# Performance work log

Hardware: AMD Instinct MI355X
Metric: run time of the kernel (lower is better)

Reference implementation:

```python
import jax, jax.numpy as jnp
import numpy as np

N_BUILD = 200000
N_COMM = 10000
E_BUILD = 1200000
E_COMM = 160000
D_B = 64    # building feature dim
D_C = 32    # community feature dim
H = 64      # hidden dim (comm embedding)
D_FUSE = D_B + H  # 128
N_CLS = 2


def gcn(x, src, dst, W, b):
    """PyG-style GCNConv with self-loops and symmetric normalization.
    out_i = sum_{j->i} h_j / sqrt(deg_j * deg_i) + h_i / deg_i + b, h = x @ W.
    deg counts in-edges plus the self-loop."""
    n = x.shape[0]
    h = x @ W                                   # [n, out]
    deg = jnp.ones((n,), x.dtype).at[dst].add(1.0)
    norm = jax.lax.rsqrt(deg)
    msg = h[src] * (norm[src] * norm[dst])[:, None]          # gather + edge weight
    agg = jax.ops.segment_sum(msg, dst, num_segments=n)      # scatter-add
    return agg + h * (1.0 / deg)[:, None] + b


def setup_inputs():
    key = jax.random.key(0)
    ks = jax.random.split(key, 24)
    f32 = jnp.float32

    def glorot(k, shape):
        scale = np.sqrt(2.0 / (shape[0] + shape[1])).astype(np.float32)
        return jax.random.normal(k, shape, dtype=f32) * scale

    inp = {
        "building_features": jax.random.normal(ks[0], (N_BUILD, D_B), dtype=f32),
        "community_features": jax.random.normal(ks[1], (N_COMM, D_C), dtype=f32),
        # GCN weights: comm 32->64->64, attention 128->2, building 128->128->64->2
        "W_c1": glorot(ks[2], (D_C, H)),   "b_c1": jnp.zeros((H,), f32),
        "W_c2": glorot(ks[3], (H, H)),     "b_c2": jnp.zeros((H,), f32),
        "W_att": glorot(ks[4], (D_FUSE, 2)), "b_att": jnp.zeros((2,), f32),
        "W_b1": glorot(ks[5], (D_FUSE, D_FUSE)), "b_b1": jnp.zeros((D_FUSE,), f32),
        "W_b2": glorot(ks[6], (D_FUSE, H)),       "b_b2": jnp.zeros((H,), f32),
        "W_b3": glorot(ks[7], (H, N_CLS)),         "b_b3": jnp.zeros((N_CLS,), f32),
        # edge lists (int) and index maps
        "b_src": jax.random.randint(ks[8], (E_BUILD,), 0, N_BUILD, dtype=jnp.int32),
        "b_dst": jax.random.randint(ks[9], (E_BUILD,), 0, N_BUILD, dtype=jnp.int32),
        "c_src": jax.random.randint(ks[10], (E_COMM,), 0, N_COMM, dtype=jnp.int32),
        "c_dst": jax.random.randint(ks[11], (E_COMM,), 0, N_COMM, dtype=jnp.int32),
        "building_to_comm_mapping": jax.random.randint(ks[12], (N_BUILD,), 0, N_COMM, dtype=jnp.int32),
        # Batch.from_data_list ordering: here identity permutation of buildings
        "local_to_global": jnp.arange(N_BUILD, dtype=jnp.int32),
    }
    return inp


def reference(building_features, community_features,
              W_c1, b_c1, W_c2, b_c2, W_att, b_att,
              W_b1, b_b1, W_b2, b_b2, W_b3, b_b3,
              b_src, b_dst, c_src, c_dst,
              building_to_comm_mapping, local_to_global):
    # Community GNN (dropout is identity in eval)
    comm_x = jax.nn.relu(gcn(community_features, c_src, c_dst, W_c1, b_c1))
    comm_x = jax.nn.relu(gcn(comm_x, c_src, c_dst, W_c2, b_c2))

    # Irregular gather: per-building community embedding
    building_comm = comm_x[building_to_comm_mapping]          # [N_build, H]

    # Feature attention: softmax gate over the two modalities
    logits = jnp.concatenate([building_features, building_comm], axis=1) @ W_att + b_att
    a = jax.nn.softmax(logits, axis=1)                        # [N_build, 2]
    fused = jnp.concatenate([building_features * a[:, 0:1],
                             building_comm * a[:, 1:2]], axis=1)  # [N_build, 128]

    # Batched building GNN over disjoint per-community subgraphs
    local_x = fused[local_to_global]
    x = jax.nn.relu(gcn(local_x, b_src, b_dst, W_b1, b_b1))
    x = jax.nn.relu(gcn(x, b_src, b_dst, W_b2, b_b2))
    x = gcn(x, b_src, b_dst, W_b3, b_b3)                      # [N_build, 2]

    # Scatter back to global order, then log-softmax
    combined = jnp.zeros((building_features.shape[0], N_CLS), x.dtype)
    combined = combined.at[local_to_global].set(x)
    return jax.nn.log_softmax(combined, axis=1)
```

## Files before the change

### kernel.cpp

```cpp
#include <hip/hip_runtime.h>
#include <hip/hip_bf16.h>
#include <math.h>

#define N_BUILD 200000
#define N_COMM  10000
#define E_BUILD 1200000
#define E_COMM  160000
#define NB_B 196
#define NB_C 10
#define CHUNK 2048
#define CB_B ((E_BUILD + CHUNK - 1) / CHUNK)
#define CB_C ((E_COMM  + CHUNK - 1) / CHUNK)

typedef __bf16 bf16x8 __attribute__((ext_vector_type(8)));
typedef float  f32x4  __attribute__((ext_vector_type(4)));

__device__ __forceinline__ unsigned short f2b(float f) {
    unsigned int u = __builtin_bit_cast(unsigned int, f);
    u += 0x7fffu + ((u >> 16) & 1u);
    return (unsigned short)(u >> 16);
}
__device__ __forceinline__ float b2f(unsigned short h) {
    unsigned int u = ((unsigned int)h) << 16;
    return __builtin_bit_cast(float, u);
}
__device__ __forceinline__ unsigned int pk2(float a, float b) {
    return (unsigned int)f2b(a) | ((unsigned int)f2b(b) << 16);
}
__device__ __forceinline__ void up8(uint4 v, float* r) {
    r[0] = b2f((unsigned short)v.x); r[1] = b2f((unsigned short)(v.x >> 16));
    r[2] = b2f((unsigned short)v.y); r[3] = b2f((unsigned short)(v.y >> 16));
    r[4] = b2f((unsigned short)v.z); r[5] = b2f((unsigned short)(v.z >> 16));
    r[6] = b2f((unsigned short)v.w); r[7] = b2f((unsigned short)(v.w >> 16));
}

#define INIT_TOT (N_BUILD + N_COMM + 2 * N_BUILD + N_COMM * 32 + 2048 + 4096 + 16384 + 8192)
__global__ __launch_bounds__(256) void init_k(int* cnt_b, int* cnt_c, float* out,
                                              const float* __restrict__ cF, unsigned short* __restrict__ cFb,
                                              const float* __restrict__ W_c1, unsigned short* __restrict__ Wt_c1,
                                              const float* __restrict__ W_c2, unsigned short* __restrict__ Wt_c2,
                                              const float* __restrict__ W_b1, unsigned short* __restrict__ Wt_b1,
                                              const float* __restrict__ W_b2, unsigned short* __restrict__ Wt_b2) {
    int i = blockIdx.x * blockDim.x + threadIdx.x;
    if (i < N_BUILD) { cnt_b[i] = 0; return; }
    i -= N_BUILD;
    if (i < N_COMM) { cnt_c[i] = 0; return; }
    i -= N_COMM;
    if (i < 2 * N_BUILD) { out[i] = -0.69314718056f; return; }
    i -= 2 * N_BUILD;
    if (i < N_COMM * 32) { cFb[i] = f2b(cF[i]); return; }
    i -= N_COMM * 32;
    if (i < 2048) { Wt_c1[(i % 64) * 32 + i / 64] = f2b(W_c1[i]); return; }
    i -= 2048;
    if (i < 4096) { Wt_c2[(i % 64) * 64 + i / 64] = f2b(W_c2[i]); return; }
    i -= 4096;
    if (i < 16384) { Wt_b1[(i % 128) * 128 + i / 128] = f2b(W_b1[i]); return; }
    i -= 16384;
    if (i < 8192) { Wt_b2[(i % 64) * 128 + i / 64] = f2b(W_b2[i]); }
}


__global__ __launch_bounds__(256) void hist2_k(int* cnt_b, const int* __restrict__ b_dst,
                                               int* cnt_c, const int* __restrict__ c_dst) {
    int i = blockIdx.x * blockDim.x + threadIdx.x;
    if (i < E_BUILD) atomicAdd(&cnt_b[b_dst[i]], 1);
    else if (i < E_BUILD + E_COMM) atomicAdd(&cnt_c[c_dst[i - E_BUILD]], 1);
}

__global__ __launch_bounds__(256) void scan1m_k(const int* __restrict__ cnt_b, int* __restrict__ ex_b, int* __restrict__ bs_b,
                                                const int* __restrict__ cnt_c, int* __restrict__ ex_c, int* __restrict__ bs_c) {
    __shared__ int sdata[256];
    const int tid = threadIdx.x;
    const int* cnt; int* ex; int* bs; int n, blk;
    if ((int)blockIdx.x < NB_B) { cnt = cnt_b; ex = ex_b; bs = bs_b; n = N_BUILD; blk = blockIdx.x; }
    else                        { cnt = cnt_c; ex = ex_c; bs = bs_c; n = N_COMM;  blk = blockIdx.x - NB_B; }
    const int base = blk * 1024 + tid * 4;
    int v[4]; int s = 0;
#pragma unroll
    for (int j = 0; j < 4; ++j) { v[j] = (base + j < n) ? cnt[base + j] : 0; s += v[j]; }
    sdata[tid] = s; __syncthreads();
    for (int off = 1; off < 256; off <<= 1) {
        int t = (tid >= off) ? sdata[tid - off] : 0;
        __syncthreads();
        sdata[tid] += t;
        __syncthreads();
    }
    if (tid == 255) bs[blk] = sdata[255];
    int run = sdata[tid] - s;
#pragma unroll
    for (int j = 0; j < 4; ++j) { if (base + j < n) ex[base + j] = run; run += v[j]; }
}

__global__ __launch_bounds__(256) void scan2m_k(int* bs_b, int* bs_c) {
    __shared__ int sdata[256];
    int* bs = (blockIdx.x == 0) ? bs_b : bs_c;
    int nb  = (blockIdx.x == 0) ? NB_B : NB_C;
    const int tid = threadIdx.x;
    int v = (tid < nb) ? bs[tid] : 0;
    sdata[tid] = v; __syncthreads();
    for (int off = 1; off < 256; off <<= 1) {
        int t = (tid >= off) ? sdata[tid - off] : 0;
        __syncthreads();
        sdata[tid] += t;
        __syncthreads();
    }
    if (tid < nb) bs[tid] = sdata[tid] - v;
}

__global__ __launch_bounds__(256) void finalizem_k(const int* __restrict__ cnt_b, int* rp_b, const int* __restrict__ bo_b,
                                                   int* cur_b, float* di_b,
                                                   const int* __restrict__ cnt_c, int* rp_c, const int* __restrict__ bo_c,
                                                   int* cur_c, float* di_c) {
    int i = blockIdx.x * blockDim.x + threadIdx.x;
    if (i < N_BUILD) {
        int cc = cnt_b[i];
        int r = rp_b[i] + bo_b[i >> 10];
        rp_b[i] = r; cur_b[i] = r; di_b[i] = 1.0f / (float)(cc + 1);
        if (i == 0) { rp_b[N_BUILD] = E_BUILD; rp_c[N_COMM] = E_COMM; }
    } else if (i < N_BUILD + N_COMM) {
        int ic = i - N_BUILD;
        int cc = cnt_c[ic];
        int r = rp_c[ic] + bo_c[ic >> 10];
        rp_c[ic] = r; cur_c[ic] = r; di_c[ic] = 1.0f / (float)(cc + 1);
    }
}

template<int NDIV>
__device__ __forceinline__ void scatter_part(const int* __restrict__ src, const int* __restrict__ dst,
                                             int* cur, const float* __restrict__ di,
                                             int2* __restrict__ cse, int E, int cid, int x) {
    int base = cid * CHUNK + threadIdx.x;
#pragma unroll
    for (int j = 0; j < CHUNK / 256; ++j, base += 256) {
        if (base < E) {
            int d = dst[base];
            if ((unsigned)d / (unsigned)NDIV == (unsigned)x) {
                int s = src[base];
                int pos = atomicAdd(&cur[d], 1);
                cse[pos] = make_int2(s, __float_as_int(sqrtf(di[s] * di[d])));
            }
        }
    }
}

__global__ __launch_bounds__(256) void csr_scatterp_k(const int* __restrict__ b_src, const int* __restrict__ b_dst,
                                                      int* cur_b, const float* __restrict__ di_b, int2* __restrict__ cse_b,
                                                      const int* __restrict__ c_src, const int* __restrict__ c_dst,
                                                      int* cur_c, const float* __restrict__ di_c, int2* __restrict__ cse_c) {
    int bid = blockIdx.x;
    if (bid < 8 * CB_B) {
        scatter_part<N_BUILD / 8>(b_src, b_dst, cur_b, di_b, cse_b, E_BUILD, bid >> 3, bid & 7);
    } else {
        bid -= 8 * CB_B;
        scatter_part<N_COMM / 8>(c_src, c_dst, cur_c, di_c, cse_c, E_COMM, bid >> 3, bid & 7);
    }
}

template<int K, int N, bool GUARD>
__global__ __launch_bounds__(256) void gemm_mfma_k(const unsigned short* __restrict__ X,
                                                   const unsigned short* __restrict__ Wt,
                                                   unsigned short* __restrict__ H, int M) {
    constexpr int GPR = K / 8;
    __shared__ unsigned short sA[64 * K];
    __shared__ unsigned short sB[N * K];
    const int tid  = threadIdx.x;
    const int row0 = blockIdx.x * 64;

    for (int idx = tid; idx < 64 * GPR; idx += 256) {
        int r = idx / GPR, g = idx % GPR;
        uint4 v = make_uint4(0u, 0u, 0u, 0u);
        if (!GUARD || row0 + r < M)
            v = *(const uint4*)&X[(size_t)(row0 + r) * K + g * 8];
        int gs = g ^ (r & (GPR - 1));
        *(uint4*)&sA[r * K + gs * 8] = v;
    }
    for (int idx = tid; idx < N * GPR; idx += 256) {
        int r = idx / GPR, g = idx % GPR;
        uint4 v = *(const uint4*)&Wt[(size_t)r * K + g * 8];
        int gs = g ^ (r & (GPR - 1));
        *(uint4*)&sB[r * K + gs * 8] = v;
    }
    __syncthreads();

    const int wave = tid >> 6, lane = tid & 63;
    const int rA = wave * 16 + (lane & 15);
    const int kg = lane >> 4;

    f32x4 zero = {0.f, 0.f, 0.f, 0.f};
    f32x4 acc[N / 16];
#pragma unroll
    for (int t = 0; t < N / 16; ++t) acc[t] = zero;

#pragma unroll
    for (int ks = 0; ks < K / 32; ++ks) {
        int gA = (ks * 4 + kg) ^ (rA & (GPR - 1));
        bf16x8 a = *(const bf16x8*)&sA[rA * K + gA * 8];
#pragma unroll
        for (int t = 0; t < N / 16; ++t) {
            int rB = t * 16 + (lane & 15);
            int gB = (ks * 4 + kg) ^ (rB & (GPR - 1));
            bf16x8 b = *(const bf16x8*)&sB[rB * K + gB * 8];
            acc[t] = __builtin_amdgcn_mfma_f32_16x16x32_bf16(a, b, acc[t], 0, 0, 0);
        }
    }

    const int crow = wave * 16 + (lane >> 4) * 4;
    const int ccol = lane & 15;
#pragma unroll
    for (int t = 0; t < N / 16; ++t) {
#pragma unroll
        for (int j = 0; j < 4; ++j) {
            int r = row0 + crow + j;
            if (!GUARD || r < M)
                H[(size_t)r * N + t * 16 + ccol] = f2b(acc[t][j]);
        }
    }
}

__global__ __launch_bounds__(256) void gemm_att_k(const float* __restrict__ bF,
                                                  const unsigned short* __restrict__ cx,
                                                  const int* __restrict__ map,
                                                  const int* __restrict__ l2g,
                                                  const float* __restrict__ Watt,
                                                  const float* __restrict__ batt,
                                                  const unsigned short* __restrict__ Wt,
                                                  unsigned short* __restrict__ H) {
    constexpr int K = 128, N = 128, GPR = 16;
    __shared__ unsigned short sA[64 * K];
    __shared__ unsigned short sB[N * K];
    __shared__ float sWt[256];
    const int tid = threadIdx.x;
    const int row0 = blockIdx.x * 64;
    sWt[tid] = Watt[tid];
    for (int idx = tid; idx < N * GPR; idx += 256) {
        int r = idx / GPR, g = idx % GPR;
        uint4 v = *(const uint4*)&Wt[(size_t)r * K + g * 8];
        int gs = g ^ (r & (GPR - 1));
        *(uint4*)&sB[r * K + gs * 8] = v;
    }
    __syncthreads();
    {
        const int r = tid >> 2, j = tid & 3;
        const int g = l2g[row0 + r];
        float vals[32];
        if (j < 2) {
            const float* f1 = &bF[(size_t)g * 64 + j * 32];
#pragma unroll
            for (int t = 0; t < 8; ++t) {
                float4 v = *(const float4*)&f1[t * 4];
                vals[t*4+0]=v.x; vals[t*4+1]=v.y; vals[t*4+2]=v.z; vals[t*4+3]=v.w;
            }
        } else {
            const unsigned short* f2 = &cx[(size_t)map[g] * 64 + (j & 1) * 32];
#pragma unroll
            for (int t = 0; t < 4; ++t) {
                uint4 u = *(const uint4*)&f2[t * 8];
                up8(u, &vals[t * 8]);
            }
        }
        float l0 = 0.f, l1 = 0.f;
        const int ch0 = j * 32;
#pragma unroll
        for (int t = 0; t < 32; ++t) {
            l0 = fmaf(vals[t], sWt[(ch0 + t) * 2 + 0], l0);
            l1 = fmaf(vals[t], sWt[(ch0 + t) * 2 + 1], l1);
        }
        l0 += __shfl_xor(l0, 1, 4); l0 += __shfl_xor(l0, 2, 4);
        l1 += __shfl_xor(l1, 1, 4); l1 += __shfl_xor(l1, 2, 4);
        l0 += batt[0]; l1 += batt[1];
        float mm = fmaxf(l0, l1);
        float e0 = __expf(l0 - mm), e1 = __expf(l1 - mm);
        float a = ((j < 2) ? e0 : e1) / (e0 + e1);
#pragma unroll
        for (int t = 0; t < 4; ++t) {
            uint4 o;
            o.x = pk2(vals[t*8+0]*a, vals[t*8+1]*a);
            o.y = pk2(vals[t*8+2]*a, vals[t*8+3]*a);
            o.z = pk2(vals[t*8+4]*a, vals[t*8+5]*a);
            o.w = pk2(vals[t*8+6]*a, vals[t*8+7]*a);
            int gi = j * 4 + t;
            int gs = gi ^ (r & (GPR - 1));
            *(uint4*)&sA[r * K + gs * 8] = o;
        }
    }
    __syncthreads();
    const int wave = tid >> 6, lane = tid & 63;
    const int rA = wave * 16 + (lane & 15);
    const int kg = lane >> 4;
    f32x4 zero = {0.f, 0.f, 0.f, 0.f};
    f32x4 acc[8];
#pragma unroll
    for (int t = 0; t < 8; ++t) acc[t] = zero;
#pragma unroll
    for (int ks = 0; ks < 4; ++ks) {
        int gA = (ks * 4 + kg) ^ (rA & 15);
        bf16x8 a = *(const bf16x8*)&sA[rA * K + gA * 8];
#pragma unroll
        for (int t = 0; t < 8; ++t) {
            int rB = t * 16 + (lane & 15);
            int gB = (ks * 4 + kg) ^ (rB & 15);
            bf16x8 b = *(const bf16x8*)&sB[rB * K + gB * 8];
            acc[t] = __builtin_amdgcn_mfma_f32_16x16x32_bf16(a, b, acc[t], 0, 0, 0);
        }
    }
    const int crow = wave * 16 + (lane >> 4) * 4;
    const int ccol = lane & 15;
#pragma unroll
    for (int t = 0; t < 8; ++t)
#pragma unroll
        for (int jj = 0; jj < 4; ++jj)
            H[(size_t)(row0 + crow + jj) * N + t * 16 + ccol] = f2b(acc[t][jj]);
}

template<int F, bool RELU>
__global__ __launch_bounds__(256) void gatherF_k(const int* __restrict__ rowptr,
                                                 const int2* __restrict__ cse,
                                                 const unsigned short* __restrict__ h,
                                                 const float* __restrict__ dinv,
                                                 const float* __restrict__ bias,
                                                 unsigned short* __restrict__ out, int nGrp) {
    constexpr int LPN = F / 8;
    constexpr int NPW = 64 / LPN;
    int wid = (blockIdx.x * blockDim.x + threadIdx.x) >> 6;
    int lane = threadIdx.x & 63;
    if (wid >= nGrp) return;
    int node = wid * NPW + lane / LPN;
    int c = (lane % LPN) * 8;
    int beg = rowptr[node], end = rowptr[node + 1];
    uint4 hv = *(const uint4*)&h[(size_t)node * F + c];
    float iv = dinv[node];
    float4 bb0 = *(const float4*)&bias[c];
    float4 bb1 = *(const float4*)&bias[c + 4];
    float acc[8];
#pragma unroll
    for (int i = 0; i < 8; ++i) acc[i] = 0.f;
    for (int p = beg; p < end; p += 8) {
        int2 q[8]; uint4 v[8];
#pragma unroll
        for (int t = 0; t < 8; ++t) { int e = p + t; q[t] = cse[e < end ? e : 0]; }
#pragma unroll
        for (int t = 0; t < 8; ++t) v[t] = *(const uint4*)&h[(size_t)q[t].x * F + c];
#pragma unroll
        for (int t = 0; t < 8; ++t) {
            float w = (p + t < end) ? __int_as_float(q[t].y) : 0.f;
            float r[8]; up8(v[t], r);
#pragma unroll
            for (int i = 0; i < 8; ++i) acc[i] = fmaf(r[i], w, acc[i]);
        }
    }
    float hr[8]; up8(hv, hr);
    float o[8];
    o[0] = fmaf(hr[0], iv, acc[0]) + bb0.x; o[1] = fmaf(hr[1], iv, acc[1]) + bb0.y;
    o[2] = fmaf(hr[2], iv, acc[2]) + bb0.z; o[3] = fmaf(hr[3], iv, acc[3]) + bb0.w;
    o[4] = fmaf(hr[4], iv, acc[4]) + bb1.x; o[5] = fmaf(hr[5], iv, acc[5]) + bb1.y;
    o[6] = fmaf(hr[6], iv, acc[6]) + bb1.z; o[7] = fmaf(hr[7], iv, acc[7]) + bb1.w;
    if (RELU) {
#pragma unroll
        for (int i = 0; i < 8; ++i) o[i] = fmaxf(o[i], 0.f);
    }
    uint4 ov;
    ov.x = pk2(o[0], o[1]); ov.y = pk2(o[2], o[3]);
    ov.z = pk2(o[4], o[5]); ov.w = pk2(o[6], o[7]);
    *(uint4*)&out[(size_t)node * F + c] = ov;
}

__global__ __launch_bounds__(256) void gather64_dot_k(const int* __restrict__ rowptr,
                                                      const int2* __restrict__ cse,
                                                      const unsigned short* __restrict__ h,
                                                      const float* __restrict__ dinv,
                                                      const float* __restrict__ bias,
                                                      const float* __restrict__ W3,
                                                      float* __restrict__ Dh, int nOct) {
    int wid = (blockIdx.x * blockDim.x + threadIdx.x) >> 6;
    int lane = threadIdx.x & 63;
    if (wid >= nOct) return;
    int node = wid * 8 + (lane >> 3);
    int sl = lane & 7, c = sl * 8;
    int beg = rowptr[node], end = rowptr[node + 1];
    uint4 hv = *(const uint4*)&h[(size_t)node * 64 + c];
    float iv = dinv[node];
    float4 bb0 = *(const float4*)&bias[c];
    float4 bb1 = *(const float4*)&bias[c + 4];
    float4 w4[4];
#pragma unroll
    for (int i = 0; i < 4; ++i) w4[i] = *(const float4*)&W3[c * 2 + i * 4];
    float acc[8];
#pragma unroll
    for (int i = 0; i < 8; ++i) acc[i] = 0.f;
    for (int p = beg; p < end; p += 8) {
        int2 q[8]; uint4 v[8];
#pragma unroll
        for (int t = 0; t < 8; ++t) { int e = p + t; q[t] = cse[e < end ? e : 0]; }
#pragma unroll
        for (int t = 0; t < 8; ++t) v[t] = *(const uint4*)&h[(size_t)q[t].x * 64 + c];
#pragma unroll
        for (int t = 0; t < 8; ++t) {
            float w = (p + t < end) ? __int_as_float(q[t].y) : 0.f;
            float r[8]; up8(v[t], r);
#pragma unroll
            for (int i = 0; i < 8; ++i) acc[i] = fmaf(r[i], w, acc[i]);
        }
    }
    float hr[8]; up8(hv, hr);
    float o[8];
    o[0] = fmaf(hr[0], iv, acc[0]) + bb0.x; o[1] = fmaf(hr[1], iv, acc[1]) + bb0.y;
    o[2] = fmaf(hr[2], iv, acc[2]) + bb0.z; o[3] = fmaf(hr[3], iv, acc[3]) + bb0.w;
    o[4] = fmaf(hr[4], iv, acc[4]) + bb1.x; o[5] = fmaf(hr[5], iv, acc[5]) + bb1.y;
    o[6] = fmaf(hr[6], iv, acc[6]) + bb1.z; o[7] = fmaf(hr[7], iv, acc[7]) + bb1.w;
#pragma unroll
    for (int i = 0; i < 8; ++i) o[i] = fmaxf(o[i], 0.f);
    float d0 = 0.f, d1 = 0.f;
#pragma unroll
    for (int i = 0; i < 4; ++i) {
        d0 = fmaf(o[2*i],   w4[i].x, d0); d0 = fmaf(o[2*i+1], w4[i].z, d0);
        d1 = fmaf(o[2*i],   w4[i].y, d1); d1 = fmaf(o[2*i+1], w4[i].w, d1);
    }
#pragma unroll
    for (int m = 1; m < 8; m <<= 1) {
        d0 += __shfl_xor(d0, m, 8);
        d1 += __shfl_xor(d1, m, 8);
    }
    if (sl == 0) {
        Dh[2 * (size_t)node + 0] = d0;
        Dh[2 * (size_t)node + 1] = d1;
    }
}

__global__ __launch_bounds__(256) void gather2_logsm_k(const int* __restrict__ rowptr,
                                                       const int2* __restrict__ cse,
                                                       const float* __restrict__ h2,
                                                       const float* __restrict__ dinv,
                                                       const float* __restrict__ bias,
                                                       const int* __restrict__ l2g,
                                                       float* __restrict__ out, int n) {
    int i = blockIdx.x * blockDim.x + threadIdx.x;
    if (i >= n) return;
    int beg = rowptr[i], end = rowptr[i + 1];
    float2 hv = *(const float2*)&h2[2 * (size_t)i];
    float iv = dinv[i];
    float a = 0.f, b = 0.f;
    for (int p = beg; p < end; p += 8) {
        int2 q[8]; float2 v[8];
#pragma unroll
        for (int t = 0; t < 8; ++t) { int e = p + t; q[t] = cse[e < end ? e : 0]; }
#pragma unroll
        for (int t = 0; t < 8; ++t) v[t] = *(const float2*)&h2[2 * (size_t)q[t].x];
#pragma unroll
        for (int t = 0; t < 8; ++t) {
            float w = (p + t < end) ? __int_as_float(q[t].y) : 0.f;
            a = fmaf(v[t].x, w, a);
            b = fmaf(v[t].y, w, b);
        }
    }
    a = fmaf(hv.x, iv, a) + bias[0];
    b = fmaf(hv.y, iv, b) + bias[1];
    float m = fmaxf(a, b);
    float ls = m + logf(__expf(a - m) + __expf(b - m));
    int g = l2g[i];
    out[2 * (size_t)g + 0] = a - ls;
    out[2 * (size_t)g + 1] = b - ls;
}


static inline dim3 g1(long long n, int tpb = 256) { return dim3((unsigned)((n + tpb - 1) / tpb)); }

extern "C" void kernel_launch(void* const* d_in, const int* in_sizes, int n_in,
                              void* d_out, int out_size, void* d_ws, size_t ws_size,
                              hipStream_t stream) {
    const float* bF   = (const float*)d_in[0];
    const float* cF   = (const float*)d_in[1];
    const float* W_c1 = (const float*)d_in[2];
    const float* b_c1 = (const float*)d_in[3];
    const float* W_c2 = (const float*)d_in[4];
    const float* b_c2 = (const float*)d_in[5];
    const float* W_at = (const float*)d_in[6];
    const float* b_at = (const float*)d_in[7];
    const float* W_b1 = (const float*)d_in[8];
    const float* b_b1 = (const float*)d_in[9];
    const float* W_b2 = (const float*)d_in[10];
    const float* b_b2 = (const float*)d_in[11];
    const float* W_b3 = (const float*)d_in[12];
    const float* b_b3 = (const float*)d_in[13];
    const int* b_src = (const int*)d_in[14];
    const int* b_dst = (const int*)d_in[15];
    const int* c_src = (const int*)d_in[16];
    const int* c_dst = (const int*)d_in[17];
    const int* map   = (const int*)d_in[18];
    const int* l2g   = (const int*)d_in[19];
    float* out = (float*)d_out;

    char* p = (char*)d_ws;
    auto alloc = [&](size_t bytes) { char* q = p; p += (bytes + 15) & ~(size_t)15; return q; };
    int*   cnt_b    = (int*)  alloc(N_BUILD * 4);
    int*   rowptr_b = (int*)  alloc((N_BUILD + 4) * 4);
    int*   cursor_b = (int*)  alloc(N_BUILD * 4);
    int*   bsum_b   = (int*)  alloc(256 * 4);
    int*   cnt_c    = (int*)  alloc(N_COMM * 4);
    int*   rowptr_c = (int*)  alloc((N_COMM + 4) * 4);
    int*   cursor_c = (int*)  alloc(N_COMM * 4);
    int*   bsum_c   = (int*)  alloc(256 * 4);
    int2*  cse_b    = (int2*) alloc((size_t)E_BUILD * 8);
    int2*  cse_c    = (int2*) alloc((size_t)E_COMM * 8);
    float* dinv_b   = (float*)alloc(N_BUILD * 4);
    float* dinv_c   = (float*)alloc(N_COMM * 4);
    unsigned short* cFb    = (unsigned short*)alloc((size_t)N_COMM * 32 * 2);
    unsigned short* Wt_c1  = (unsigned short*)alloc(64 * 32 * 2);
    unsigned short* Wt_c2  = (unsigned short*)alloc(64 * 64 * 2);
    unsigned short* Wt_b1  = (unsigned short*)alloc(128 * 128 * 2);
    unsigned short* Wt_b2  = (unsigned short*)alloc(64 * 128 * 2);
    unsigned short* ch_bf  = (unsigned short*)alloc((size_t)N_COMM * 64 * 2);
    unsigned short* cx1_bf = (unsigned short*)alloc((size_t)N_COMM * 64 * 2);
    unsigned short* cx2_bf = (unsigned short*)alloc((size_t)N_COMM * 64 * 2);
    unsigned short* A_bf   = (unsigned short*)alloc((size_t)N_BUILD * 128 * 2);
    unsigned short* B_bf   = (unsigned short*)alloc((size_t)N_BUILD * 128 * 2);
    float* Dh = (float*)alloc((size_t)N_BUILD * 2 * 4);

    init_k<<<g1(INIT_TOT), 256, 0, stream>>>(cnt_b, cnt_c, out,
                                             cF, cFb, W_c1, Wt_c1, W_c2, Wt_c2, W_b1, Wt_b1, W_b2, Wt_b2);
    hist2_k<<<g1(E_BUILD + E_COMM), 256, 0, stream>>>(cnt_b, b_dst, cnt_c, c_dst);
    scan1m_k<<<NB_B + NB_C, 256, 0, stream>>>(cnt_b, rowptr_b, bsum_b, cnt_c, rowptr_c, bsum_c);
    scan2m_k<<<2, 256, 0, stream>>>(bsum_b, bsum_c);
    finalizem_k<<<g1(N_BUILD + N_COMM), 256, 0, stream>>>(cnt_b, rowptr_b, bsum_b, cursor_b, dinv_b,
                                                          cnt_c, rowptr_c, bsum_c, cursor_c, dinv_c);
    csr_scatterp_k<<<8 * (CB_B + CB_C), 256, 0, stream>>>(b_src, b_dst, cursor_b, dinv_b, cse_b,
                                                          c_src, c_dst, cursor_c, dinv_c, cse_c);

    gemm_mfma_k<32, 64, true><<<dim3((N_COMM + 63) / 64), 256, 0, stream>>>(cFb, Wt_c1, ch_bf, N_COMM);
    gatherF_k<64, true><<<g1((long long)(N_COMM / 8) * 64), 256, 0, stream>>>(rowptr_c, cse_c, ch_bf, dinv_c, b_c1, cx1_bf, N_COMM / 8);

    gemm_mfma_k<64, 64, true><<<dim3((N_COMM + 63) / 64), 256, 0, stream>>>(cx1_bf, Wt_c2, ch_bf, N_COMM);
    gatherF_k<64, true><<<g1((long long)(N_COMM / 8) * 64), 256, 0, stream>>>(rowptr_c, cse_c, ch_bf, dinv_c, b_c2, cx2_bf, N_COMM / 8);

    gemm_att_k<<<dim3(N_BUILD / 64), 256, 0, stream>>>(bF, cx2_bf, map, l2g, W_at, b_at, Wt_b1, B_bf);
    gatherF_k<128, true><<<g1((long long)(N_BUILD / 4) * 64), 256, 0, stream>>>(rowptr_b, cse_b, B_bf, dinv_b, b_b1, A_bf, N_BUILD / 4);

    gemm_mfma_k<128, 64, false><<<dim3(N_BUILD / 64), 256, 0, stream>>>(A_bf, Wt_b2, B_bf, N_BUILD);
    gather64_dot_k<<<g1((long long)(N_BUILD / 8) * 64), 256, 0, stream>>>(rowptr_b, cse_b, B_bf, dinv_b, b_b2, W_b3, Dh, N_BUILD / 8);

    gather2_logsm_k<<<g1(N_BUILD), 256, 0, stream>>>(rowptr_b, cse_b, Dh, dinv_b, b_b3, l2g, out, N_BUILD);
}
```

Baseline: 338.9 us.

## Aggregate before first building GEMM and fuse layer-1 and layer-2 GEMMs

Uses the linearity of GCN aggregation: layer 1 now aggregates the attention-scaled fused input (A·X) before multiplying by W_b1, instead of aggregating X·W_b1. The aggregation reads building features compacted to bf16 plus a per-node community index and attention weights, and forms the 128-wide fused row on the fly. The community half is gathered from the small 10k-row embedding table rather than from a materialised 128-channel H. The first-layer GEMM with bias and ReLU and the second-layer GEMM are then fused into one MFMA kernel that keeps the intermediate in LDS, removing one 200k×128 round trip through global memory. In exchange there is an extra small attention kernel and indirect loads of afus and mbl per edge in the aggregation.

```diff
diff --git a/kernel.cpp b/kernel.cpp
--- a/kernel.cpp
+++ b/kernel.cpp
@@ -217,99 +217,205 @@
     }
 }
 
-__global__ __launch_bounds__(256) void gemm_att_k(const float* __restrict__ bF,
-                                                  const unsigned short* __restrict__ cx,
-                                                  const int* __restrict__ map,
-                                                  const int* __restrict__ l2g,
-                                                  const float* __restrict__ Watt,
-                                                  const float* __restrict__ batt,
-                                                  const unsigned short* __restrict__ Wt,
-                                                  unsigned short* __restrict__ H) {
-    constexpr int K = 128, N = 128, GPR = 16;
+__global__ __launch_bounds__(256) void attscal_k(const float* __restrict__ bF,
+                                                 const unsigned short* __restrict__ cx,
+                                                 const int* __restrict__ map,
+                                                 const int* __restrict__ l2g,
+                                                 const float* __restrict__ Watt,
+                                                 const float* __restrict__ batt,
+                                                 unsigned short* __restrict__ bFl,
+                                                 float2* __restrict__ afus,
+                                                 int* __restrict__ mbl, int n) {
+    __shared__ float sW0[128], sW1[128];
+    if (threadIdx.x < 128) {
+        sW0[threadIdx.x] = Watt[threadIdx.x * 2 + 0];
+        sW1[threadIdx.x] = Watt[threadIdx.x * 2 + 1];
+    }
+    __syncthreads();
+    int gid = blockIdx.x * blockDim.x + threadIdx.x;
+    int i = gid >> 3, j = gid & 7;
+    if (i >= n) return;
+    int g = l2g[i];
+    int mg = map[g];
+    const float* f1 = &bF[(size_t)g * 64 + j * 8];
+    const unsigned short* f2 = &cx[(size_t)mg * 64 + j * 8];
+    float r1[8], r2[8];
+    {
+        float4 v0 = *(const float4*)&f1[0];
+        float4 v1 = *(const float4*)&f1[4];
+        r1[0]=v0.x; r1[1]=v0.y; r1[2]=v0.z; r1[3]=v0.w;
+        r1[4]=v1.x; r1[5]=v1.y; r1[6]=v1.z; r1[7]=v1.w;
+        uint4 u = *(const uint4*)&f2[0];
+        up8(u, r2);
+    }
+    float l0 = 0.f, l1 = 0.f;
+#pragma unroll
+    for (int k = 0; k < 8; ++k) {
+        l0 = fmaf(r1[k], sW0[j * 8 + k], l0);
+        l1 = fmaf(r1[k], sW1[j * 8 + k], l1);
+        l0 = fmaf(r2[k], sW0[64 + j * 8 + k], l0);
+        l1 = fmaf(r2[k], sW1[64 + j * 8 + k], l1);
+    }
+#pragma unroll
+    for (int m = 1; m < 8; m <<= 1) {
+        l0 += __shfl_xor(l0, m, 8);
+        l1 += __shfl_xor(l1, m, 8);
+    }
+    l0 += batt[0]; l1 += batt[1];
+    float mm = fmaxf(l0, l1);
+    float e0 = __expf(l0 - mm), e1 = __expf(l1 - mm);
+    float inv = 1.0f / (e0 + e1);
+    uint4 o;
+    o.x = pk2(r1[0], r1[1]); o.y = pk2(r1[2], r1[3]);
+    o.z = pk2(r1[4], r1[5]); o.w = pk2(r1[6], r1[7]);
+    *(uint4*)&bFl[(size_t)i * 64 + j * 8] = o;
+    if (j == 0) {
+        afus[i] = make_float2(e0 * inv, e1 * inv);
+        mbl[i] = mg;
+    }
+}
+
+__global__ __launch_bounds__(256) void agg1_k(const int* __restrict__ rowptr,
+                                              const int2* __restrict__ cse,
+                                              const unsigned short* __restrict__ bFl,
+                                              const unsigned short* __restrict__ cx2,
+                                              const int* __restrict__ mbl,
+                                              const float2* __restrict__ afus,
+                                              const float* __restrict__ dinv,
+                                              unsigned short* __restrict__ y1,
+                                              int nGrp) {
+    int wid = (blockIdx.x * blockDim.x + threadIdx.x) >> 6;
+    int lane = threadIdx.x & 63;
+    if (wid >= nGrp) return;
+    int node = wid * 4 + (lane >> 4);
+    int sl = lane & 15;
+    bool upper = sl >= 8;
+    int c = (sl & 7) * 8;
+    int beg = rowptr[node], end = rowptr[node + 1];
+    float2 afi = afus[node];
+    int mbi = mbl[node];
+    uint4 hv = upper ? *(const uint4*)&cx2[(size_t)mbi * 64 + c]
+                     : *(const uint4*)&bFl[(size_t)node * 64 + c];
+    float selfw = dinv[node] * (upper ? afi.y : afi.x);
+    float acc[8];
+#pragma unroll
+    for (int i = 0; i < 8; ++i) acc[i] = 0.f;
+    for (int p = beg; p < end; p += 8) {
+        int2 q[8];
+#pragma unroll
+        for (int t = 0; t < 8; ++t) { int e = p + t; q[t] = cse[e < end ? e : 0]; }
+        float2 af[8]; int mb[8];
+#pragma unroll
+        for (int t = 0; t < 8; ++t) { af[t] = afus[q[t].x]; mb[t] = mbl[q[t].x]; }
+        uint4 v[8];
+#pragma unroll
+        for (int t = 0; t < 8; ++t) {
+            const unsigned short* base = upper ? &cx2[(size_t)mb[t] * 64 + c]
+                                               : &bFl[(size_t)q[t].x * 64 + c];
+            v[t] = *(const uint4*)base;
+        }
+#pragma unroll
+        for (int t = 0; t < 8; ++t) {
+            float w = (p + t < end) ? __int_as_float(q[t].y) : 0.f;
+            float wa = w * (upper ? af[t].y : af[t].x);
+            float r[8]; up8(v[t], r);
+#pragma unroll
+            for (int i = 0; i < 8; ++i) acc[i] = fmaf(r[i], wa, acc[i]);
+        }
+    }
+    float hr[8]; up8(hv, hr);
+#pragma unroll
+    for (int i = 0; i < 8; ++i) acc[i] = fmaf(hr[i], selfw, acc[i]);
+    uint4 ov;
+    ov.x = pk2(acc[0], acc[1]); ov.y = pk2(acc[2], acc[3]);
+    ov.z = pk2(acc[4], acc[5]); ov.w = pk2(acc[6], acc[7]);
+    *(uint4*)&y1[(size_t)node * 128 + sl * 8] = ov;
+}
+
+__global__ __launch_bounds__(256) void gemm2x_k(const unsigned short* __restrict__ y1,
+                                                const unsigned short* __restrict__ Wt1,
+                                                const float* __restrict__ b1,
+                                                const unsigned short* __restrict__ Wt2,
+                                                unsigned short* __restrict__ H) {
+    constexpr int K = 128, GPR = 16;
     __shared__ unsigned short sA[64 * K];
-    __shared__ unsigned short sB[N * K];
-    __shared__ float sWt[256];
+    __shared__ unsigned short sB1[128 * K];
+    __shared__ unsigned short sB2[64 * K];
     const int tid = threadIdx.x;
     const int row0 = blockIdx.x * 64;
-    sWt[tid] = Watt[tid];
-    for (int idx = tid; idx < N * GPR; idx += 256) {
+    for (int idx = tid; idx < 64 * GPR; idx += 256) {
         int r = idx / GPR, g = idx % GPR;
-        uint4 v = *(const uint4*)&Wt[(size_t)r * K + g * 8];
+        uint4 v = *(const uint4*)&y1[(size_t)(row0 + r) * K + g * 8];
         int gs = g ^ (r & (GPR - 1));
-        *(uint4*)&sB[r * K + gs * 8] = v;
-    }
-    __syncthreads();
-    {
-        const int r = tid >> 2, j = tid & 3;
-        const int g = l2g[row0 + r];
-        float vals[32];
-        if (j < 2) {
-            const float* f1 = &bF[(size_t)g * 64 + j * 32];
-#pragma unroll
-            for (int t = 0; t < 8; ++t) {
-                float4 v = *(const float4*)&f1[t * 4];
-                vals[t*4+0]=v.x; vals[t*4+1]=v.y; vals[t*4+2]=v.z; vals[t*4+3]=v.w;
-            }
-        } else {
-            const unsigned short* f2 = &cx[(size_t)map[g] * 64 + (j & 1) * 32];
-#pragma unroll
-            for (int t = 0; t < 4; ++t) {
-                uint4 u = *(const uint4*)&f2[t * 8];
-                up8(u, &vals[t * 8]);
-            }
-        }
-        float l0 = 0.f, l1 = 0.f;
-        const int ch0 = j * 32;
-#pragma unroll
-        for (int t = 0; t < 32; ++t) {
-            l0 = fmaf(vals[t], sWt[(ch0 + t) * 2 + 0], l0);
-            l1 = fmaf(vals[t], sWt[(ch0 + t) * 2 + 1], l1);
-        }
-        l0 += __shfl_xor(l0, 1, 4); l0 += __shfl_xor(l0, 2, 4);
-        l1 += __shfl_xor(l1, 1, 4); l1 += __shfl_xor(l1, 2, 4);
-        l0 += batt[0]; l1 += batt[1];
-        float mm = fmaxf(l0, l1);
-        float e0 = __expf(l0 - mm), e1 = __expf(l1 - mm);
-        float a = ((j < 2) ? e0 : e1) / (e0 + e1);
-#pragma unroll
-        for (int t = 0; t < 4; ++t) {
-            uint4 o;
-            o.x = pk2(vals[t*8+0]*a, vals[t*8+1]*a);
-            o.y = pk2(vals[t*8+2]*a, vals[t*8+3]*a);
-            o.z = pk2(vals[t*8+4]*a, vals[t*8+5]*a);
-            o.w = pk2(vals[t*8+6]*a, vals[t*8+7]*a);
-            int gi = j * 4 + t;
-            int gs = gi ^ (r & (GPR - 1));
-            *(uint4*)&sA[r * K + gs * 8] = o;
-        }
+        *(uint4*)&sA[r * K + gs * 8] = v;
+    }
+    for (int idx = tid; idx < 128 * GPR; idx += 256) {
+        int r = idx / GPR, g = idx % GPR;
+        uint4 v = *(const uint4*)&Wt1[(size_t)r * K + g * 8];
+        int gs = g ^ (r & (GPR - 1));
+        *(uint4*)&sB1[r * K + gs * 8] = v;
+    }
+    for (int idx = tid; idx < 64 * GPR; idx += 256) {
+        int r = idx / GPR, g = idx % GPR;
+        uint4 v = *(const uint4*)&Wt2[(size_t)r * K + g * 8];
+        int gs = g ^ (r & (GPR - 1));
+        *(uint4*)&sB2[r * K + gs * 8] = v;
     }
     __syncthreads();
     const int wave = tid >> 6, lane = tid & 63;
     const int rA = wave * 16 + (lane & 15);
     const int kg = lane >> 4;
+    const int crow = wave * 16 + (lane >> 4) * 4;
+    const int ccol = lane & 15;
     f32x4 zero = {0.f, 0.f, 0.f, 0.f};
-    f32x4 acc[8];
-#pragma unroll
-    for (int t = 0; t < 8; ++t) acc[t] = zero;
+    f32x4 acc1[8];
+#pragma unroll
+    for (int t = 0; t < 8; ++t) acc1[t] = zero;
 #pragma unroll
     for (int ks = 0; ks < 4; ++ks) {
-        int gA = (ks * 4 + kg) ^ (rA & 15);
+        int gA = (ks * 4 + kg) ^ (rA & (GPR - 1));
         bf16x8 a = *(const bf16x8*)&sA[rA * K + gA * 8];
 #pragma unroll
         for (int t = 0; t < 8; ++t) {
             int rB = t * 16 + (lane & 15);
-            int gB = (ks * 4 + kg) ^ (rB & 15);
-            bf16x8 b = *(const bf16x8*)&sB[rB * K + gB * 8];
-            acc[t] = __builtin_amdgcn_mfma_f32_16x16x32_bf16(a, b, acc[t], 0, 0, 0);
-        }
-    }
-    const int crow = wave * 16 + (lane >> 4) * 4;
-    const int ccol = lane & 15;
-#pragma unroll
-    for (int t = 0; t < 8; ++t)
+            int gB = (ks * 4 + kg) ^ (rB & (GPR - 1));
+            bf16x8 b = *(const bf16x8*)&sB1[rB * K + gB * 8];
+            acc1[t] = __builtin_amdgcn_mfma_f32_16x16x32_bf16(a, b, acc1[t], 0, 0, 0);
+        }
+    }
+    __syncthreads();
+#pragma unroll
+    for (int t = 0; t < 8; ++t) {
+        float bv = b1[t * 16 + ccol];
+#pragma unroll
+        for (int j = 0; j < 4; ++j) {
+            float x = fmaxf(acc1[t][j] + bv, 0.f);
+            int r = crow + j;
+            int ch = t * 16 + ccol;
+            sA[r * K + (((ch >> 3) ^ (r & (GPR - 1))) << 3) + (ch & 7)] = f2b(x);
+        }
+    }
+    __syncthreads();
+    f32x4 acc2[4];
+#pragma unroll
+    for (int t = 0; t < 4; ++t) acc2[t] = zero;
+#pragma unroll
+    for (int ks = 0; ks < 4; ++ks) {
+        int gA = (ks * 4 + kg) ^ (rA & (GPR - 1));
+        bf16x8 a = *(const bf16x8*)&sA[rA * K + gA * 8];
+#pragma unroll
+        for (int t = 0; t < 4; ++t) {
+            int rB = t * 16 + (lane & 15);
+            int gB = (ks * 4 + kg) ^ (rB & (GPR - 1));
+            bf16x8 b = *(const bf16x8*)&sB2[rB * K + gB * 8];
+            acc2[t] = __builtin_amdgcn_mfma_f32_16x16x32_bf16(a, b, acc2[t], 0, 0, 0);
+        }
+    }
+#pragma unroll
+    for (int t = 0; t < 4; ++t)
 #pragma unroll
         for (int jj = 0; jj < 4; ++jj)
-            H[(size_t)(row0 + crow + jj) * N + t * 16 + ccol] = f2b(acc[t][jj]);
+            H[(size_t)(row0 + crow + jj) * 64 + t * 16 + ccol] = f2b(acc2[t][jj]);
 }
 
 template<int F, bool RELU>
@@ -511,8 +617,11 @@
     unsigned short* ch_bf  = (unsigned short*)alloc((size_t)N_COMM * 64 * 2);
     unsigned short* cx1_bf = (unsigned short*)alloc((size_t)N_COMM * 64 * 2);
     unsigned short* cx2_bf = (unsigned short*)alloc((size_t)N_COMM * 64 * 2);
-    unsigned short* A_bf   = (unsigned short*)alloc((size_t)N_BUILD * 128 * 2);
-    unsigned short* B_bf   = (unsigned short*)alloc((size_t)N_BUILD * 128 * 2);
+    unsigned short* bFl    = (unsigned short*)alloc((size_t)N_BUILD * 64 * 2);
+    float2* afus           = (float2*)        alloc((size_t)N_BUILD * 8);
+    int*    mbl            = (int*)           alloc((size_t)N_BUILD * 4);
+    unsigned short* y1_bf  = (unsigned short*)alloc((size_t)N_BUILD * 128 * 2);
+    unsigned short* h2_bf  = (unsigned short*)alloc((size_t)N_BUILD * 64 * 2);
     float* Dh = (float*)alloc((size_t)N_BUILD * 2 * 4);
 
     init_k<<<g1(INIT_TOT), 256, 0, stream>>>(cnt_b, cnt_c, out,
@@ -531,11 +640,15 @@
     gemm_mfma_k<64, 64, true><<<dim3((N_COMM + 63) / 64), 256, 0, stream>>>(cx1_bf, Wt_c2, ch_bf, N_COMM);
     gatherF_k<64, true><<<g1((long long)(N_COMM / 8) * 64), 256, 0, stream>>>(rowptr_c, cse_c, ch_bf, dinv_c, b_c2, cx2_bf, N_COMM / 8);
 
-    gemm_att_k<<<dim3(N_BUILD / 64), 256, 0, stream>>>(bF, cx2_bf, map, l2g, W_at, b_at, Wt_b1, B_bf);
-    gatherF_k<128, true><<<g1((long long)(N_BUILD / 4) * 64), 256, 0, stream>>>(rowptr_b, cse_b, B_bf, dinv_b, b_b1, A_bf, N_BUILD / 4);
-
-    gemm_mfma_k<128, 64, false><<<dim3(N_BUILD / 64), 256, 0, stream>>>(A_bf, Wt_b2, B_bf, N_BUILD);
-    gather64_dot_k<<<g1((long long)(N_BUILD / 8) * 64), 256, 0, stream>>>(rowptr_b, cse_b, B_bf, dinv_b, b_b2, W_b3, Dh, N_BUILD / 8);
+    attscal_k<<<g1((long long)N_BUILD * 8), 256, 0, stream>>>(bF, cx2_bf, map, l2g, W_at, b_at,
+                                                              bFl, afus, mbl, N_BUILD);
+
+    agg1_k<<<g1((long long)(N_BUILD / 4) * 64), 256, 0, stream>>>(rowptr_b, cse_b, bFl, cx2_bf, mbl, afus,
+                                                                  dinv_b, y1_bf, N_BUILD / 4);
+
+    gemm2x_k<<<dim3(N_BUILD / 64), 256, 0, stream>>>(y1_bf, Wt_b1, b_b1, Wt_b2, h2_bf);
+
+    gather64_dot_k<<<g1((long long)(N_BUILD / 8) * 64), 256, 0, stream>>>(rowptr_b, cse_b, h2_bf, dinv_b, b_b2, W_b3, Dh, N_BUILD / 8);
 
     gather2_logsm_k<<<g1(N_BUILD), 256, 0, stream>>>(rowptr_b, cse_b, Dh, dinv_b, b_b3, l2g, out, N_BUILD);
 }
```

Result: slower. 356.3 us (+5.2%).
